# Kernel tuning notes

Hardware: AMD Instinct MI355X
Metric: run time of the kernel (lower is better)

Reference implementation:

```python
import jax, jax.numpy as jnp
import numpy as np

INP, OUP, KSIZE, STRIDE = 256, 256, 3, 1
M, G = 2, 2
INP_GAP = max(16, INP // 16)  # 16
PAD = KSIZE // 2


def setup_inputs() -> dict:
    key = jax.random.key(0)
    k1, k2, k3, k4, k5 = jax.random.split(key, 5)
    B, H, W = 32, 28, 28
    x = jax.random.normal(k1, (B, INP, H, W), dtype=jnp.float32)
    x_gap = jax.random.normal(k2, (B, INP_GAP, 1, 1), dtype=jnp.float32)
    # wn_fc1: Conv2d(INP_GAP, M*OUP, 1, bias=True) -> dense [M*OUP, INP_GAP]
    w1 = jax.random.normal(k3, (M * OUP, INP_GAP), dtype=jnp.float32) * 0.1
    b1 = jax.random.normal(k4, (M * OUP,), dtype=jnp.float32) * 0.1
    # wn_fc2: grouped 1x1 conv, groups = G*OUP, 1 in-channel per group
    # -> weight is effectively a vector of length OUP*INP*KSIZE*KSIZE
    w2 = jax.random.normal(k5, (OUP * INP * KSIZE * KSIZE,), dtype=jnp.float32) * 0.05
    return {"x": x, "x_gap": x_gap, "w1": w1, "b1": b1, "w2": w2}


def reference(x, x_gap, w1, b1, w2):
    B, _, H, W = x.shape
    # fc1 (1x1 conv on [B, INP_GAP, 1, 1]) + sigmoid -> [B, M*OUP]
    h = jax.nn.sigmoid(jnp.einsum('bi,oi->bo', x_gap[:, :, 0, 0], w1) + b1)
    # fc2: groups = G*OUP, one input channel per group, INP*K*K/G outputs per group
    per = INP * KSIZE * KSIZE // G
    # [B, G*OUP, per] -> per-sample kernels [B*OUP, INP, K, K]
    wk = (w2.reshape(G * OUP, per) * h[:, :, None]).reshape(B * OUP, INP, KSIZE, KSIZE)
    # batched dynamic conv via feature_group_count = B
    y = jax.lax.conv_general_dilated(
        x.reshape(1, B * INP, H, W), wk,
        window_strides=(STRIDE, STRIDE),
        padding=[(PAD, PAD), (PAD, PAD)],
        dimension_numbers=('NCHW', 'OIHW', 'NCHW'),
        feature_group_count=B)
    return y.reshape(B, OUP, y.shape[2], y.shape[3])
```

## Files before the change

kernel.cpp:

```cpp
#include <hip/hip_runtime.h>
#include <hip/hip_bf16.h>

typedef __attribute__((ext_vector_type(8))) short bf16x8;
typedef __attribute__((ext_vector_type(4))) float f32x4;

#define NB 32
#define NO 256
#define XS_BYTES (6 * 30 * 512)

static __device__ __forceinline__ void gld16(const void* g, void* l) {
    __builtin_amdgcn_global_load_lds(
        (const __attribute__((address_space(1))) void*)g,
        (__attribute__((address_space(3))) void*)l, 16, 0, 0);
}

__global__ void prep_kernel(const float* __restrict__ w2, __hip_bfloat16* __restrict__ wrt,
                            const float* __restrict__ x, __hip_bfloat16* __restrict__ xp) {
    if (blockIdx.x < 288) {
        int idx = blockIdx.x * 256 + threadIdx.x;
        int kcol = idx & 15;
        int klo = (idx >> 4) & 3;
        int mf = (idx >> 6) & 3;
        int mw = (idx >> 8) & 3;
        int kw2 = (idx >> 10) & 1;
        int s = idx >> 11;
        int tap = s >> 2;
        int ic = s & 3;
        int o = mw * 64 + mf * 16 + kcol;
        int ch = kw2 * 128 + ic * 32 + klo * 8;
        const float* src = w2 + (size_t)o * 2304 + (size_t)ch * 9 + tap;
        union { bf16x8 v; __hip_bfloat16 e[8]; } u;
#pragma unroll
        for (int e = 0; e < 8; ++e) u.e[e] = __float2bfloat16(src[e * 9]);
        *(bf16x8*)((short*)wrt + (size_t)idx * 8) = u.v;
        return;
    }
    __shared__ float tile[64][29];
    int blk = blockIdx.x - 288;
    int icnk = blk & 3;
    int t = blk >> 2;
    int pr = t % 30;
    int b = t / 30;
    int i0 = icnk * 64;
    __hip_bfloat16* dst = xp + ((size_t)(b * 30 + pr) * 30) * 256 + i0;
    const bf16x8 z = (bf16x8){0, 0, 0, 0, 0, 0, 0, 0};
    if (pr == 0 || pr == 29) {
        for (int e = threadIdx.x; e < 30 * 8; e += 256) {
            int q = e >> 3, part = e & 7;
            *(bf16x8*)((short*)(dst + (size_t)q * 256) + part * 8) = z;
        }
        return;
    }
    int p = pr - 1;
    for (int e = threadIdx.x; e < 64 * 28; e += 256) {
        int ii = e / 28, q = e % 28;
        tile[ii][q] = x[((b * 256 + i0 + ii) * 28 + p) * 28 + q];
    }
    __syncthreads();
    for (int e = threadIdx.x; e < 28 * 64; e += 256) {
        int q = e >> 6, ii = e & 63;
        dst[(size_t)(q + 1) * 256 + ii] = __float2bfloat16(tile[ii][q]);
    }
    if (threadIdx.x < 16) {
        int col = (threadIdx.x >> 3) * 29, part = threadIdx.x & 7;
        *(bf16x8*)((short*)(dst + (size_t)col * 256) + part * 8) = z;
    }
}

#define MM(A_, B_, mf_, nf_) \
    acc[mf_][nf_] = __builtin_amdgcn_mfma_f32_16x16x32_bf16(A_, B_, acc[mf_][nf_], 0, 0, 0);

#define CLUSTER(A0, A1, A2, A3, B0, B1, B2, B3, B4, B5, B6)             \
    __builtin_amdgcn_s_setprio(1);                                      \
    MM(A0, B0, 0, 0) MM(A1, B0, 1, 0) MM(A2, B0, 2, 0) MM(A3, B0, 3, 0) \
    MM(A0, B1, 0, 1) MM(A1, B1, 1, 1) MM(A2, B1, 2, 1) MM(A3, B1, 3, 1) \
    MM(A0, B2, 0, 2) MM(A1, B2, 1, 2) MM(A2, B2, 2, 2) MM(A3, B2, 3, 2) \
    MM(A0, B3, 0, 3) MM(A1, B3, 1, 3) MM(A2, B3, 2, 3) MM(A3, B3, 3, 3) \
    MM(A0, B4, 0, 4) MM(A1, B4, 1, 4) MM(A2, B4, 2, 4) MM(A3, B4, 3, 4) \
    MM(A0, B5, 0, 5) MM(A1, B5, 1, 5) MM(A2, B5, 2, 5) MM(A3, B5, 3, 5) \
    MM(A0, B6, 0, 6) MM(A1, B6, 1, 6) MM(A2, B6, 2, 6) MM(A3, B6, 3, 6) \
    __builtin_amdgcn_s_setprio(0);

#define LOADB(D0, D1, D2, D3, D4, D5, D6, XO)                                  \
    D0 = *(const bf16x8*)(Xs + ((u[0] ^ ((kk[0] & 7u) << 4)) ^ (XO)));         \
    D1 = *(const bf16x8*)(Xs + ((u[1] ^ ((kk[1] & 7u) << 4)) ^ (XO)));         \
    D2 = *(const bf16x8*)(Xs + ((u[2] ^ ((kk[2] & 7u) << 4)) ^ (XO)));         \
    D3 = *(const bf16x8*)(Xs + ((u[3] ^ ((kk[3] & 7u) << 4)) ^ (XO)));         \
    D4 = *(const bf16x8*)(Xs + ((u[4] ^ ((kk[4] & 7u) << 4)) ^ (XO)));         \
    D5 = *(const bf16x8*)(Xs + ((u[5] ^ ((kk[5] & 7u) << 4)) ^ (XO)));         \
    D6 = *(const bf16x8*)(Xs + ((u[6] ^ ((kk[6] & 7u) << 4)) ^ (XO)));

#define PHASE(ICV, XOv)                                                       \
    {                                                                         \
        asm volatile("s_waitcnt vmcnt(4)" ::: "memory");                      \
        const char* ar = AbR + (((ICV) & 1) * 4096);                          \
        bf16x8 a0 = *(const bf16x8*)(ar);                                     \
        bf16x8 a1 = *(const bf16x8*)(ar + 1024);                              \
        bf16x8 a2 = *(const bf16x8*)(ar + 2048);                              \
        bf16x8 a3 = *(const bf16x8*)(ar + 3072);                              \
        char* l = AbW + (((ICV) & 1) * 4096);                                 \
        gld16(pG, l);                                                         \
        gld16(pG + 1024, l + 1024);                                           \
        gld16(pG + 2048, l + 2048);                                           \
        gld16(pG + 3072, l + 3072);                                           \
        pG += 32768;                                                          \
        bf16x8 bv0, bv1, bv2, bv3, bv4, bv5, bv6;                             \
        LOADB(bv0, bv1, bv2, bv3, bv4, bv5, bv6, XOv)                         \
        CLUSTER(a0, a1, a2, a3, bv0, bv1, bv2, bv3, bv4, bv5, bv6)            \
    }

__global__ __launch_bounds__(512, 2) void conv_kernel(
    const __hip_bfloat16* __restrict__ xp, const __hip_bfloat16* __restrict__ wrt,
    const float* __restrict__ xg, const float* __restrict__ w1,
    const float* __restrict__ b1, float* __restrict__ out) {
    __shared__ __align__(16) char Xs[XS_BYTES];
    __shared__ __align__(16) char Ab[8 * 2 * 4096];
    __shared__ float hsm[512];
    const int bid = blockIdx.x;
    const int v = (bid & 7) * 28 + (bid >> 3);
    const int b = v / 7;
    const int nt = v - b * 7;
    const int tid = threadIdx.x;
    const int lane = tid & 63;
    const int wv = tid >> 6;
    const int mw = wv & 3;
    const int kw2 = wv >> 2;
    const int kcol = lane & 15;
    const int klo = lane >> 4;

    const char* wrtc = (const char*)wrt;
    char* AbW = Ab + wv * 8192;
    const char* AbR = Ab + wv * 8192 + lane * 16;
    const char* pG = wrtc + wv * 4096 + lane * 16;

    gld16(pG, AbW);
    gld16(pG + 1024, AbW + 1024);
    gld16(pG + 2048, AbW + 2048);
    gld16(pG + 3072, AbW + 3072);
    pG += 32768;
    gld16(pG, AbW + 4096);
    gld16(pG + 1024, AbW + 4096 + 1024);
    gld16(pG + 2048, AbW + 4096 + 2048);
    gld16(pG + 3072, AbW + 4096 + 3072);
    pG += 32768;

    {
        float s = b1[tid];
        const float* g = xg + b * 16;
        const float* w = w1 + tid * 16;
#pragma unroll
        for (int c = 0; c < 16; ++c) s += g[c] * w[c];
        hsm[tid] = 1.0f / (1.0f + expf(-s));
    }

    {
        const char* src = (const char*)(xp + ((size_t)b * 900 + nt * 120) * 256);
        for (int c = tid; c < 5760; c += 512) {
            int sp = c >> 5, w = c & 31;
            int rr = sp / 30;
            int qq = sp - rr * 30;
            int key = (qq + 4 * rr) & 7;
            *(bf16x8*)(Xs + sp * 512 + ((w ^ key) << 4)) = *(const bf16x8*)(src + (size_t)c * 16);
        }
    }
    __syncthreads();

    unsigned u[7], kk[7];
#pragma unroll
    for (int nf = 0; nf < 7; ++nf) {
        int n = nf * 16 + kcol;
        int r0 = n / 28;
        int q0 = n - r0 * 28;
        u[nf] = (unsigned)((r0 * 30 + q0) * 512 + (klo << 4));
        kk[nf] = (unsigned)(q0 + 4 * r0);
    }
    const unsigned xo0 = (unsigned)((kw2 * 4 + 0) << 6);
    const unsigned xo1 = (unsigned)((kw2 * 4 + 1) << 6);
    const unsigned xo2 = (unsigned)((kw2 * 4 + 2) << 6);
    const unsigned xo3 = (unsigned)((kw2 * 4 + 3) << 6);

    f32x4 acc[4][7];
#pragma unroll
    for (int mf = 0; mf < 4; ++mf)
#pragma unroll
        for (int nf = 0; nf < 7; ++nf) acc[mf][nf] = (f32x4){0.f, 0.f, 0.f, 0.f};

    for (int tap = 0; tap < 9; ++tap) {
        PHASE(0, xo0)
        PHASE(1, xo1)
        PHASE(2, xo2)
        PHASE(3, xo3)
        if (tap < 8) {
            const int cross = (tap == 2 || tap == 5);
            const unsigned da = cross ? 28u * 512u : 512u;
            const unsigned dk = cross ? 2u : 1u;
#pragma unroll
            for (int nf = 0; nf < 7; ++nf) { u[nf] += da; kk[nf] += dk; }
        }
    }

    __syncthreads();
    float* Xf = (float*)Xs;
#pragma unroll
    for (int r2 = 0; r2 < 2; ++r2) {
        if (kw2 == 1) {
#pragma unroll
            for (int mfi = 0; mfi < 2; ++mfi) {
                const int mf = r2 * 2 + mfi;
#pragma unroll
                for (int nf = 0; nf < 7; ++nf) {
#pragma unroll
                    for (int rr = 0; rr < 4; ++rr) {
                        int o = mw * 64 + mf * 16 + klo * 4 + rr;
                        int idx = (((mw * 2 + mfi) * 7 + nf) * 4 + rr) * 64 + lane;
                        Xf[idx] = hsm[2 * o + 1] * acc[mf][nf][rr];
                    }
                }
            }
        }
        __syncthreads();
        if (kw2 == 0) {
#pragma unroll
            for (int mfi = 0; mfi < 2; ++mfi) {
                const int mf = r2 * 2 + mfi;
#pragma unroll
                for (int nf = 0; nf < 7; ++nf) {
#pragma unroll
                    for (int rr = 0; rr < 4; ++rr) {
                        int o = mw * 64 + mf * 16 + klo * 4 + rr;
                        int idx = (((mw * 2 + mfi) * 7 + nf) * 4 + rr) * 64 + lane;
                        float y = hsm[2 * o] * acc[mf][nf][rr] + Xf[idx];
                        out[((size_t)b * NO + o) * 784 + nt * 112 + nf * 16 + kcol] = y;
                    }
                }
            }
        }
        __syncthreads();
    }
}

extern "C" void kernel_launch(void* const* d_in, const int* in_sizes, int n_in,
                              void* d_out, int out_size, void* d_ws, size_t ws_size,
                              hipStream_t stream) {
    const float* x = (const float*)d_in[0];
    const float* xg = (const float*)d_in[1];
    const float* w1 = (const float*)d_in[2];
    const float* b1 = (const float*)d_in[3];
    const float* w2 = (const float*)d_in[4];
    float* out = (float*)d_out;

    char* ws = (char*)d_ws;
    __hip_bfloat16* wrt = (__hip_bfloat16*)ws;
    __hip_bfloat16* xp = (__hip_bfloat16*)(ws + 1179648);

    prep_kernel<<<288 + NB * 30 * 4, 256, 0, stream>>>(w2, wrt, x, xp);
    conv_kernel<<<224, 512, 0, stream>>>(xp, wrt, xg, w1, b1, out);
}
```

Baseline: 49.87 us.

## Software-pipeline LDS B-fragment loads one phase ahead of MFMA clusters

Double-buffers the B fragments in registers so each phase issues LDS reads for the next phase before running the MFMA cluster on the current one, with sched_barrier keeping that order. The last phase of each tap now runs after the pointer advance, so it prefetches the next tap's first fragment. This hides LDS latency behind MFMA work at the cost of seven more bf16x8 registers per lane, which could cause spills under launch_bounds(512,2). The last iteration also reads a prefetch past the final tap that is never used.

```diff
diff --git a/kernel.cpp b/kernel.cpp
--- a/kernel.cpp
+++ b/kernel.cpp
@@ -90,7 +90,7 @@
     D5 = *(const bf16x8*)(Xs + ((u[5] ^ ((kk[5] & 7u) << 4)) ^ (XO)));         \
     D6 = *(const bf16x8*)(Xs + ((u[6] ^ ((kk[6] & 7u) << 4)) ^ (XO)));
 
-#define PHASE(ICV, XOv)                                                       \
+#define PHASE_E(ICV, XON)                                                     \
     {                                                                         \
         asm volatile("s_waitcnt vmcnt(4)" ::: "memory");                      \
         const char* ar = AbR + (((ICV) & 1) * 4096);                          \
@@ -104,9 +104,27 @@
         gld16(pG + 2048, l + 2048);                                           \
         gld16(pG + 3072, l + 3072);                                           \
         pG += 32768;                                                          \
-        bf16x8 bv0, bv1, bv2, bv3, bv4, bv5, bv6;                             \
-        LOADB(bv0, bv1, bv2, bv3, bv4, bv5, bv6, XOv)                         \
-        CLUSTER(a0, a1, a2, a3, bv0, bv1, bv2, bv3, bv4, bv5, bv6)            \
+        LOADB(bn0, bn1, bn2, bn3, bn4, bn5, bn6, XON)                         \
+        __builtin_amdgcn_sched_barrier(0);                                    \
+        CLUSTER(a0, a1, a2, a3, bc0, bc1, bc2, bc3, bc4, bc5, bc6)            \
+    }
+#define PHASE_O(ICV, XON)                                                     \
+    {                                                                         \
+        asm volatile("s_waitcnt vmcnt(4)" ::: "memory");                      \
+        const char* ar = AbR + (((ICV) & 1) * 4096);                          \
+        bf16x8 a0 = *(const bf16x8*)(ar);                                     \
+        bf16x8 a1 = *(const bf16x8*)(ar + 1024);                              \
+        bf16x8 a2 = *(const bf16x8*)(ar + 2048);                              \
+        bf16x8 a3 = *(const bf16x8*)(ar + 3072);                              \
+        char* l = AbW + (((ICV) & 1) * 4096);                                 \
+        gld16(pG, l);                                                         \
+        gld16(pG + 1024, l + 1024);                                           \
+        gld16(pG + 2048, l + 2048);                                           \
+        gld16(pG + 3072, l + 3072);                                           \
+        pG += 32768;                                                          \
+        LOADB(bc0, bc1, bc2, bc3, bc4, bc5, bc6, XON)                         \
+        __builtin_amdgcn_sched_barrier(0);                                    \
+        CLUSTER(a0, a1, a2, a3, bn0, bn1, bn2, bn3, bn4, bn5, bn6)            \
     }
 
 __global__ __launch_bounds__(512, 2) void conv_kernel(
@@ -185,11 +203,14 @@
 #pragma unroll
         for (int nf = 0; nf < 7; ++nf) acc[mf][nf] = (f32x4){0.f, 0.f, 0.f, 0.f};
 
+    bf16x8 bc0, bc1, bc2, bc3, bc4, bc5, bc6;
+    bf16x8 bn0, bn1, bn2, bn3, bn4, bn5, bn6;
+    LOADB(bc0, bc1, bc2, bc3, bc4, bc5, bc6, xo0)
+
     for (int tap = 0; tap < 9; ++tap) {
-        PHASE(0, xo0)
-        PHASE(1, xo1)
-        PHASE(2, xo2)
-        PHASE(3, xo3)
+        PHASE_E(0, xo1)
+        PHASE_O(1, xo2)
+        PHASE_E(2, xo3)
         if (tap < 8) {
             const int cross = (tap == 2 || tap == 5);
             const unsigned da = cross ? 28u * 512u : 512u;
@@ -197,6 +218,7 @@
 #pragma unroll
             for (int nf = 0; nf < 7; ++nf) { u[nf] += da; kk[nf] += dk; }
         }
+        PHASE_O(3, xo0)
     }
 
     __syncthreads();
```

New measurement: 49.94 us. About the same (+0.1%).

## Software-pipeline LDS operand loads with register double-buffering across MFMA phases

Applied to the files above, without the earlier changes.

The main loop is restructured so that the next phase's A-fragment and B-fragment LDS reads, plus the global-to-LDS prefetch, are issued between two halves of the current phase's MFMA cluster. Two register sets (A and B variants) alternate across phases, with a prologue before the loop and a sched_barrier to keep the ordering. The goal is to hide LDS read latency behind MFMA execution instead of stalling before each cluster. In exchange it needs many more live VGPRs (22 extra bf16x8 fragments), which risks spills or lower occupancy under launch_bounds(512,2). It also issues one extra prefetch past the last phase.

```diff
diff --git a/kernel.cpp b/kernel.cpp
--- a/kernel.cpp
+++ b/kernel.cpp
@@ -70,12 +70,15 @@
 #define MM(A_, B_, mf_, nf_) \
     acc[mf_][nf_] = __builtin_amdgcn_mfma_f32_16x16x32_bf16(A_, B_, acc[mf_][nf_], 0, 0, 0);
 
-#define CLUSTER(A0, A1, A2, A3, B0, B1, B2, B3, B4, B5, B6)             \
+#define CL_H1(A0, A1, A2, A3, B0, B1, B2, B3)                           \
     __builtin_amdgcn_s_setprio(1);                                      \
     MM(A0, B0, 0, 0) MM(A1, B0, 1, 0) MM(A2, B0, 2, 0) MM(A3, B0, 3, 0) \
     MM(A0, B1, 0, 1) MM(A1, B1, 1, 1) MM(A2, B1, 2, 1) MM(A3, B1, 3, 1) \
     MM(A0, B2, 0, 2) MM(A1, B2, 1, 2) MM(A2, B2, 2, 2) MM(A3, B2, 3, 2) \
     MM(A0, B3, 0, 3) MM(A1, B3, 1, 3) MM(A2, B3, 2, 3) MM(A3, B3, 3, 3) \
+    __builtin_amdgcn_s_setprio(0);
+#define CL_H2(A0, A1, A2, A3, B4, B5, B6)                               \
+    __builtin_amdgcn_s_setprio(1);                                      \
     MM(A0, B4, 0, 4) MM(A1, B4, 1, 4) MM(A2, B4, 2, 4) MM(A3, B4, 3, 4) \
     MM(A0, B5, 0, 5) MM(A1, B5, 1, 5) MM(A2, B5, 2, 5) MM(A3, B5, 3, 5) \
     MM(A0, B6, 0, 6) MM(A1, B6, 1, 6) MM(A2, B6, 2, 6) MM(A3, B6, 3, 6) \
@@ -90,23 +93,39 @@
     D5 = *(const bf16x8*)(Xs + ((u[5] ^ ((kk[5] & 7u) << 4)) ^ (XO)));         \
     D6 = *(const bf16x8*)(Xs + ((u[6] ^ ((kk[6] & 7u) << 4)) ^ (XO)));
 
-#define PHASE(ICV, XOv)                                                       \
+#define PHASE_E(BUFOFF, XON)                                                  \
     {                                                                         \
+        CL_H1(aA0, aA1, aA2, aA3, bA0, bA1, bA2, bA3)                         \
         asm volatile("s_waitcnt vmcnt(4)" ::: "memory");                      \
-        const char* ar = AbR + (((ICV) & 1) * 4096);                          \
-        bf16x8 a0 = *(const bf16x8*)(ar);                                     \
-        bf16x8 a1 = *(const bf16x8*)(ar + 1024);                              \
-        bf16x8 a2 = *(const bf16x8*)(ar + 2048);                              \
-        bf16x8 a3 = *(const bf16x8*)(ar + 3072);                              \
-        char* l = AbW + (((ICV) & 1) * 4096);                                 \
-        gld16(pG, l);                                                         \
-        gld16(pG + 1024, l + 1024);                                           \
-        gld16(pG + 2048, l + 2048);                                           \
-        gld16(pG + 3072, l + 3072);                                           \
+        aB0 = *(const bf16x8*)(AbR + (BUFOFF));                               \
+        aB1 = *(const bf16x8*)(AbR + (BUFOFF) + 1024);                        \
+        aB2 = *(const bf16x8*)(AbR + (BUFOFF) + 2048);                        \
+        aB3 = *(const bf16x8*)(AbR + (BUFOFF) + 3072);                        \
+        gld16(pG, AbW + (BUFOFF));                                            \
+        gld16(pG + 1024, AbW + (BUFOFF) + 1024);                              \
+        gld16(pG + 2048, AbW + (BUFOFF) + 2048);                              \
+        gld16(pG + 3072, AbW + (BUFOFF) + 3072);                              \
         pG += 32768;                                                          \
-        bf16x8 bv0, bv1, bv2, bv3, bv4, bv5, bv6;                             \
-        LOADB(bv0, bv1, bv2, bv3, bv4, bv5, bv6, XOv)                         \
-        CLUSTER(a0, a1, a2, a3, bv0, bv1, bv2, bv3, bv4, bv5, bv6)            \
+        LOADB(bB0, bB1, bB2, bB3, bB4, bB5, bB6, XON)                         \
+        __builtin_amdgcn_sched_barrier(0);                                    \
+        CL_H2(aA0, aA1, aA2, aA3, bA4, bA5, bA6)                              \
+    }
+#define PHASE_O(BUFOFF, XON)                                                  \
+    {                                                                         \
+        CL_H1(aB0, aB1, aB2, aB3, bB0, bB1, bB2, bB3)                         \
+        asm volatile("s_waitcnt vmcnt(4)" ::: "memory");                      \
+        aA0 = *(const bf16x8*)(AbR + (BUFOFF));                               \
+        aA1 = *(const bf16x8*)(AbR + (BUFOFF) + 1024);                        \
+        aA2 = *(const bf16x8*)(AbR + (BUFOFF) + 2048);                        \
+        aA3 = *(const bf16x8*)(AbR + (BUFOFF) + 3072);                        \
+        gld16(pG, AbW + (BUFOFF));                                            \
+        gld16(pG + 1024, AbW + (BUFOFF) + 1024);                              \
+        gld16(pG + 2048, AbW + (BUFOFF) + 2048);                              \
+        gld16(pG + 3072, AbW + (BUFOFF) + 3072);                              \
+        pG += 32768;                                                          \
+        LOADB(bA0, bA1, bA2, bA3, bA4, bA5, bA6, XON)                         \
+        __builtin_amdgcn_sched_barrier(0);                                    \
+        CL_H2(aB0, aB1, aB2, aB3, bB4, bB5, bB6)                              \
     }
 
 __global__ __launch_bounds__(512, 2) void conv_kernel(
@@ -185,11 +204,25 @@
 #pragma unroll
         for (int nf = 0; nf < 7; ++nf) acc[mf][nf] = (f32x4){0.f, 0.f, 0.f, 0.f};
 
+    bf16x8 aA0, aA1, aA2, aA3, aB0, aB1, aB2, aB3;
+    bf16x8 bA0, bA1, bA2, bA3, bA4, bA5, bA6;
+    bf16x8 bB0, bB1, bB2, bB3, bB4, bB5, bB6;
+
+    aA0 = *(const bf16x8*)(AbR);
+    aA1 = *(const bf16x8*)(AbR + 1024);
+    aA2 = *(const bf16x8*)(AbR + 2048);
+    aA3 = *(const bf16x8*)(AbR + 3072);
+    gld16(pG, AbW);
+    gld16(pG + 1024, AbW + 1024);
+    gld16(pG + 2048, AbW + 2048);
+    gld16(pG + 3072, AbW + 3072);
+    pG += 32768;
+    LOADB(bA0, bA1, bA2, bA3, bA4, bA5, bA6, xo0)
+
     for (int tap = 0; tap < 9; ++tap) {
-        PHASE(0, xo0)
-        PHASE(1, xo1)
-        PHASE(2, xo2)
-        PHASE(3, xo3)
+        PHASE_E(4096, xo1)
+        PHASE_O(0, xo2)
+        PHASE_E(4096, xo3)
         if (tap < 8) {
             const int cross = (tap == 2 || tap == 5);
             const unsigned da = cross ? 28u * 512u : 512u;
@@ -197,6 +230,7 @@
 #pragma unroll
             for (int nf = 0; nf < 7; ++nf) { u[nf] += da; kk[nf] += dk; }
         }
+        PHASE_O(0, xo0)
     }
 
     __syncthreads();
```

After: 49.72 us. No clear change (-0.3%).
